# Kernel optimization log

Measured on AMD Instinct MI355X. Metric: run time of the kernel, lower is better.

The kernel has to match this reference:

```python
import jax, jax.numpy as jnp
import numpy as np
from jax import lax

FEATURE_NUM = 16
FILTERS = 64
BATCH = 64
WINDOW = 5
T = 2048
SECTORS = 11
D = 256          # embedding dim / number of quantization buckets
DA = 64
VOCAB = 100000
L = T - 3 * WINDOW + 3  # 2036, length after conv->maxpool->conv (all valid, stride 1)
BN_EPS = 1e-5


def _conv1d(x, w):
    # x: [N, C, W], w: [O, I, K], valid padding, stride 1
    return lax.conv_general_dilated(x, w, (1,), 'VALID', dimension_numbers=('NCH', 'OIH', 'NCH'))


def setup_inputs() -> dict:
    key = jax.random.key(0)
    ks = jax.random.split(key, 9)
    x = jax.random.normal(ks[0], (BATCH, 2 * FEATURE_NUM, T), jnp.float32)
    conv1_w = jax.random.normal(ks[1], (FILTERS, 2 * FEATURE_NUM, WINDOW), jnp.float32) * 0.1
    conv1_b = jnp.zeros((FILTERS,), jnp.float32)
    bn_gamma = jnp.ones((FILTERS,), jnp.float32)
    bn_beta = jnp.zeros((FILTERS,), jnp.float32)
    conv2_w = jax.random.normal(ks[2], (1, FILTERS, WINDOW), jnp.float32) * 0.1
    conv2_b = jnp.zeros((1,), jnp.float32)
    emb = jax.random.normal(ks[3], (VOCAB, D), jnp.float32)
    W1 = jax.random.normal(ks[4], (DA, L), jnp.float32)
    W2 = jax.random.normal(ks[5], (DA, 1), jnp.float32)
    lin_w = jax.random.normal(ks[6], (SECTORS, D), jnp.float32) * 0.05
    lin_b = jnp.zeros((SECTORS,), jnp.float32)
    return {'x': x, 'conv1_w': conv1_w, 'conv1_b': conv1_b, 'bn_gamma': bn_gamma,
            'bn_beta': bn_beta, 'conv2_w': conv2_w, 'conv2_b': conv2_b, 'emb': emb,
            'W1': W1, 'W2': W2, 'lin_w': lin_w, 'lin_b': lin_b}


def reference(x, conv1_w, conv1_b, bn_gamma, bn_beta, conv2_w, conv2_b, emb, W1, W2, lin_w, lin_b):
    # conv1 (valid) -> maxpool(k=WINDOW, s=1) -> batchnorm (train-mode batch stats) -> conv2 -> relu
    h = _conv1d(x, conv1_w) + conv1_b[None, :, None]                     # [B, F, T-W+1]
    h = lax.reduce_window(h, -jnp.inf, lax.max, (1, 1, WINDOW), (1, 1, 1), 'VALID')
    mu = jnp.mean(h, axis=(0, 2), keepdims=True)
    var = jnp.mean((h - mu) ** 2, axis=(0, 2), keepdims=True)            # biased, as torch BN train
    h = (h - mu) * lax.rsqrt(var + BN_EPS) * bn_gamma[None, :, None] + bn_beta[None, :, None]
    h = jax.nn.relu(_conv1d(h, conv2_w) + conv2_b[None, :, None])        # [B, 1, L]
    c = jax.nn.sigmoid(h[:, 0, :])                                       # [B, L] in (0,1)
    # embedding_generate: first j with c <= (j+1)/D  <=>  j = ceil(c*D) - 1
    idx = jnp.clip(jnp.ceil(c * D).astype(jnp.int32) - 1, 0, D - 1)      # [B, L]
    e = emb[idx]                                                         # [B, L, D]
    # per-sample attention: A = W2^T tanh(W1 @ out), batched as einsums
    t = jnp.tanh(jnp.einsum('al,bld->bad', W1, e))                       # [B, DA, D]
    A = jnp.einsum('a,bad->bd', W2[:, 0], t)                             # [B, D]
    att = jax.nn.softmax(jnp.einsum('bld,bd->bl', e, A), axis=1)         # [B, L]
    scores = A @ lin_w.T + lin_b                                         # [B, SECTORS]
    return att, scores
```

## Files before the change

### kernel.cpp

```cpp
#include <hip/hip_runtime.h>
#include <hip/hip_bf16.h>
#include <math.h>

#define BATCH 64
#define CIN   32
#define TIN   2048
#define FILT  64
#define WIN   5
#define TP1   2044
#define TP2   2040
#define LOUT  2036
#define DEMB  256
#define DA    64
#define NSEC  11
#define NC    4
#define CS    509
#define TILE_T 252

__global__ __launch_bounds__(256) void k_prep(
    const float* __restrict__ W1, const float* __restrict__ emb,
    const float* __restrict__ w1, float* __restrict__ w1t,
    float* __restrict__ embT, float* __restrict__ w1r, int* __restrict__ count) {
  __shared__ float tl[64 * 65];
  int bk = blockIdx.x;
  const int tid = threadIdx.x;
  if (bk < 64) { count[bk * 256 + tid] = 0; return; }
  bk -= 64;
  if (bk < 32) {
    const int l0 = bk * 64;
    const int lc = tid & 63, rq = tid >> 6;
    for (int a = rq; a < 64; a += 4)
      tl[a * 65 + lc] = (l0 + lc < LOUT) ? W1[a * LOUT + l0 + lc] : 0.f;
    __syncthreads();
    for (int lp = rq; lp < 64; lp += 4)
      if (l0 + lp < LOUT) w1t[(l0 + lp) * 64 + lc] = tl[lc * 65 + lp];
    return;
  }
  bk -= 32;
  if (bk < 16) {
    const int j0 = (bk & 3) * 64, d0 = (bk >> 2) * 64;
    const int c = tid & 63, rq = tid >> 6;
    for (int j = rq; j < 64; j += 4) tl[j * 65 + c] = emb[(j0 + j) * DEMB + d0 + c];
    __syncthreads();
    for (int d = rq; d < 64; d += 4) embT[(d0 + d) * DEMB + j0 + c] = tl[c * 65 + d];
    return;
  }
  bk -= 16;
  {
    int i = bk * 256 + tid;
    int c = i / 320, r = i - c * 320, f = r / 5, k = r - f * 5;
    w1r[i] = w1[f * (CIN * WIN) + c * WIN + k];
  }
}

__global__ __launch_bounds__(256) void k_conv1pool(
    const float* __restrict__ x, const float* __restrict__ w1r,
    const float* __restrict__ b1, float* __restrict__ h2,
    float* __restrict__ bnps, float* __restrict__ bnpq) {
  __shared__ float wl[CIN * 160];
  const int b   = blockIdx.y;
  const int t0  = blockIdx.x * TILE_T;
  const int tid = threadIdx.x;
  const int z   = blockIdx.z;

  for (int i = tid; i < CIN * 160; i += 256) {
    int c = i / 160, r = i - c * 160;
    wl[i] = w1r[c * 320 + z * 160 + r];
  }
  __syncthreads();

  const int tg   = tid & 63;
  const int tb   = tg * 4;
  const int wv40 = (tid >> 6) * 40;
  const int wf0  = __builtin_amdgcn_readfirstlane(z * 32 + (tid >> 6) * 8);

  float acc[8][4];
#pragma unroll
  for (int ff = 0; ff < 8; ++ff) {
    float bias = b1[wf0 + ff];
    acc[ff][0] = bias; acc[ff][1] = bias; acc[ff][2] = bias; acc[ff][3] = bias;
  }

  const float* xrow = x + (size_t)b * CIN * TIN + t0 + tb;
  const bool safe = (t0 + tb + 8) <= TIN;

  for (int c = 0; c < CIN; ++c) {
    float xw[8];
    if (safe) {
      float4 xa = *(const float4*)(xrow + c * TIN);
      float4 xb = *(const float4*)(xrow + c * TIN + 4);
      xw[0] = xa.x; xw[1] = xa.y; xw[2] = xa.z; xw[3] = xa.w;
      xw[4] = xb.x; xw[5] = xb.y; xw[6] = xb.z; xw[7] = xb.w;
    } else {
#pragma unroll
      for (int j = 0; j < 8; ++j) {
        int gt = t0 + tb + j;
        xw[j] = (gt < TIN) ? xrow[c * TIN + j] : 0.f;
      }
    }
    float wa[40];
#pragma unroll
    for (int q = 0; q < 10; ++q) {
      float4 wq = *(const float4*)&wl[c * 160 + wv40 + q * 4];
      wa[q * 4 + 0] = wq.x; wa[q * 4 + 1] = wq.y;
      wa[q * 4 + 2] = wq.z; wa[q * 4 + 3] = wq.w;
    }
#pragma unroll
    for (int ff = 0; ff < 8; ++ff) {
#pragma unroll
      for (int k = 0; k < WIN; ++k) {
        float wv = wa[ff * 5 + k];
        acc[ff][0] = fmaf(xw[k + 0], wv, acc[ff][0]);
        acc[ff][1] = fmaf(xw[k + 1], wv, acc[ff][1]);
        acc[ff][2] = fmaf(xw[k + 2], wv, acc[ff][2]);
        acc[ff][3] = fmaf(xw[k + 3], wv, acc[ff][3]);
      }
    }
  }

  const bool rowvalid = (tg < 63);
  const int blk = b * 9 + blockIdx.x;
#pragma unroll
  for (int ff = 0; ff < 8; ++ff) {
    float n0 = __shfl_down(acc[ff][0], 1);
    float n1 = __shfl_down(acc[ff][1], 1);
    float n2 = __shfl_down(acc[ff][2], 1);
    float n3 = __shfl_down(acc[ff][3], 1);
    float h[8] = {acc[ff][0], acc[ff][1], acc[ff][2], acc[ff][3], n0, n1, n2, n3};
    float o0 = fmaxf(fmaxf(fmaxf(h[0], h[1]), fmaxf(h[2], h[3])), h[4]);
    float o1 = fmaxf(fmaxf(fmaxf(h[1], h[2]), fmaxf(h[3], h[4])), h[5]);
    float o2 = fmaxf(fmaxf(fmaxf(h[2], h[3]), fmaxf(h[4], h[5])), h[6]);
    float o3 = fmaxf(fmaxf(fmaxf(h[3], h[4]), fmaxf(h[5], h[6])), h[7]);
    const int f = wf0 + ff;
    float s = 0.f, q = 0.f;
    const int t2b = t0 + tb;
    if (rowvalid && (t2b + 3 < TP2)) {
      *(float4*)&h2[((size_t)b * FILT + f) * TP2 + t2b] = make_float4(o0, o1, o2, o3);
      s = o0 + o1 + o2 + o3;
      q = o0 * o0 + o1 * o1 + o2 * o2 + o3 * o3;
    } else if (rowvalid) {
      float ov[4] = {o0, o1, o2, o3};
#pragma unroll
      for (int j = 0; j < 4; ++j) {
        int t2 = t2b + j;
        if (t2 < TP2) { h2[((size_t)b * FILT + f) * TP2 + t2] = ov[j]; s += ov[j]; q += ov[j] * ov[j]; }
      }
    }
#pragma unroll
    for (int off = 32; off > 0; off >>= 1) {
      s += __shfl_down(s, off);
      q += __shfl_down(q, off);
    }
    if (tg == 0) { bnps[blk * FILT + f] = s; bnpq[blk * FILT + f] = q; }
  }
}

__global__ __launch_bounds__(256) void k_bnfin(
    const float* __restrict__ bnps, const float* __restrict__ bnpq,
    const float* __restrict__ gamma, const float* __restrict__ beta,
    const float* __restrict__ w2, const float* __restrict__ b2,
    double* __restrict__ ws2, double* __restrict__ c0p) {
  __shared__ double ls[4 * 64], lq[4 * 64];
  const int tid = threadIdx.x;
  const int f = tid & 63, g = tid >> 6;
  double s = 0.0, q = 0.0;
  for (int blk = g; blk < 576; blk += 4) {
    s += (double)bnps[blk * FILT + f];
    q += (double)bnpq[blk * FILT + f];
  }
  ls[g * 64 + f] = s; lq[g * 64 + f] = q;
  __syncthreads();
  if (tid < 64) {
    s = ls[tid] + ls[64 + tid] + ls[128 + tid] + ls[192 + tid];
    q = lq[tid] + lq[64 + tid] + lq[128 + tid] + lq[192 + tid];
    const double N = (double)(BATCH * TP2);
    double mu  = s / N;
    double var = q / N - mu * mu;
    double sc  = (double)gamma[tid] / sqrt(var + 1e-5);
    double sh  = (double)beta[tid] - mu * sc;
    double wsum = 0.0;
#pragma unroll
    for (int k = 0; k < WIN; ++k) {
      double wv = (double)w2[tid * WIN + k];
      ws2[tid * WIN + k] = sc * wv;
      wsum += wv;
    }
    double part = sh * wsum;
#pragma unroll
    for (int off = 32; off > 0; off >>= 1) part += __shfl_down(part, off);
    if (tid == 0) c0p[0] = part + (double)b2[0];
  }
}

__global__ __launch_bounds__(256) void k_conv2(
    const float* __restrict__ h2, const double* __restrict__ ws2,
    const double* __restrict__ c0p, int* __restrict__ idxp, int* __restrict__ count) {
  __shared__ float hl[FILT * 260];
  __shared__ int hist[DEMB];
  const int b = blockIdx.y;
  const int t0 = blockIdx.x * 256;
  const int tid = threadIdx.x;
  for (int i = tid; i < FILT * 260; i += 256) {
    int f = i / 260, o = i - f * 260;
    int gt = t0 + o;
    hl[i] = (gt < TP2) ? h2[((size_t)b * FILT + f) * TP2 + gt] : 0.f;
  }
  hist[tid] = 0;
  __syncthreads();
  const int t = t0 + tid;
  if (t < LOUT) {
    double z = c0p[0];
    for (int f = 0; f < FILT; ++f) {
      const double* wr = ws2 + f * WIN;
      z = fma((double)hl[f * 260 + tid + 0], wr[0], z);
      z = fma((double)hl[f * 260 + tid + 1], wr[1], z);
      z = fma((double)hl[f * 260 + tid + 2], wr[2], z);
      z = fma((double)hl[f * 260 + tid + 3], wr[3], z);
      z = fma((double)hl[f * 260 + tid + 4], wr[4], z);
    }
    z = z > 0.0 ? z : 0.0;
    double c = 1.0 / (1.0 + exp(-z));
    int iv = (int)ceil(c * 256.0) - 1;
    iv = min(max(iv, 0), DEMB - 1);
    idxp[b * LOUT + t] = iv;
    atomicAdd(&hist[iv], 1);
  }
  __syncthreads();
  atomicAdd(&count[b * DEMB + tid], hist[tid]);
}

__global__ __launch_bounds__(256) void k_sbuild(
    const int* __restrict__ idxp, const float* __restrict__ w1t,
    float* __restrict__ Sg) {
  __shared__ float S[DA * 257];
  __shared__ int il[512];
  const int b = blockIdx.y, ch = blockIdx.x;
  const int tid = threadIdx.x;
  for (int i = tid; i < DA * 257; i += 256) S[i] = 0.f;
  const int l0 = ch * CS;
  for (int i = tid; i < CS; i += 256) il[i] = idxp[b * LOUT + l0 + i];
  __syncthreads();
  const int a = tid & 63, w = tid >> 6;
#pragma unroll 4
  for (int li = w; li < CS; li += 4) {
    int j = il[li];
    float v = w1t[(l0 + li) * DA + a];
    atomicAdd(&S[a * 257 + j], v);
  }
  __syncthreads();
  for (int i = tid; i < DA * DEMB; i += 256) {
    int aa = i >> 8, j = i & 255;
    Sg[((b * NC + ch) * DA + aa) * DEMB + j] = S[aa * 257 + j];
  }
}

__global__ __launch_bounds__(256) void k_gemmA(
    const float* __restrict__ Sg, const float* __restrict__ emb,
    const float* __restrict__ W2, float* __restrict__ Avec) {
  __shared__ float Al[16 * 64];
  __shared__ float Bl[16 * 64];
  __shared__ float red[16 * 64];
  const int b = blockIdx.x, c0 = blockIdx.y * 64;
  const int tid = threadIdx.x;
  const int tx = tid & 15, ty = tid >> 4;
  const int sa = tid >> 2, skq = (tid & 3) * 4;
  const int bk = tid >> 4, bseg = tid & 15;
  float acc[4][4] = {{0}};

  for (int kc = 0; kc < 16; ++kc) {
    const int kb = kc * 16;
    float4 v0 = *(const float4*)&Sg[((b * NC + 0) * DA + sa) * DEMB + kb + skq];
    float4 v1 = *(const float4*)&Sg[((b * NC + 1) * DA + sa) * DEMB + kb + skq];
    float4 v2 = *(const float4*)&Sg[((b * NC + 2) * DA + sa) * DEMB + kb + skq];
    float4 v3 = *(const float4*)&Sg[((b * NC + 3) * DA + sa) * DEMB + kb + skq];
    float4 sv = make_float4(v0.x + v1.x + v2.x + v3.x, v0.y + v1.y + v2.y + v3.y,
                            v0.z + v1.z + v2.z + v3.z, v0.w + v1.w + v2.w + v3.w);
    Al[(skq + 0) * 64 + sa] = sv.x;
    Al[(skq + 1) * 64 + sa] = sv.y;
    Al[(skq + 2) * 64 + sa] = sv.z;
    Al[(skq + 3) * 64 + sa] = sv.w;
    float4 e4 = *(const float4*)&emb[(kb + bk) * DEMB + c0 + bseg * 4];
    *(float4*)&Bl[bk * 64 + bseg * 4] = e4;
    __syncthreads();
#pragma unroll
    for (int k = 0; k < 16; ++k) {
      float4 av = *(const float4*)&Al[k * 64 + ty * 4];
      float4 bv = *(const float4*)&Bl[k * 64 + tx * 4];
      acc[0][0] = fmaf(av.x, bv.x, acc[0][0]); acc[0][1] = fmaf(av.x, bv.y, acc[0][1]);
      acc[0][2] = fmaf(av.x, bv.z, acc[0][2]); acc[0][3] = fmaf(av.x, bv.w, acc[0][3]);
      acc[1][0] = fmaf(av.y, bv.x, acc[1][0]); acc[1][1] = fmaf(av.y, bv.y, acc[1][1]);
      acc[1][2] = fmaf(av.y, bv.z, acc[1][2]); acc[1][3] = fmaf(av.y, bv.w, acc[1][3]);
      acc[2][0] = fmaf(av.z, bv.x, acc[2][0]); acc[2][1] = fmaf(av.z, bv.y, acc[2][1]);
      acc[2][2] = fmaf(av.z, bv.z, acc[2][2]); acc[2][3] = fmaf(av.z, bv.w, acc[2][3]);
      acc[3][0] = fmaf(av.w, bv.x, acc[3][0]); acc[3][1] = fmaf(av.w, bv.y, acc[3][1]);
      acc[3][2] = fmaf(av.w, bv.z, acc[3][2]); acc[3][3] = fmaf(av.w, bv.w, acc[3][3]);
    }
    __syncthreads();
  }
  float cs[4] = {0.f, 0.f, 0.f, 0.f};
#pragma unroll
  for (int r = 0; r < 4; ++r) {
    float wv = W2[ty * 4 + r];
#pragma unroll
    for (int j = 0; j < 4; ++j) cs[j] += tanhf(acc[r][j]) * wv;
  }
#pragma unroll
  for (int j = 0; j < 4; ++j) red[ty * 64 + tx * 4 + j] = cs[j];
  __syncthreads();
  if (tid < 64) {
    float s = 0.f;
#pragma unroll
    for (int q = 0; q < 16; ++q) s += red[q * 64 + tid];
    Avec[b * DEMB + c0 + tid] = s;
  }
}

__global__ __launch_bounds__(256) void k_att(
    const float* __restrict__ Avec, const float* __restrict__ embT,
    const int* __restrict__ count, const float* __restrict__ linw,
    const float* __restrict__ linb, const int* __restrict__ idxp,
    float* __restrict__ att, float* __restrict__ scores) {
  __shared__ float Al[DEMB];
  __shared__ float pl[DEMB];
  __shared__ float scratch[4];
  const int b = blockIdx.x, j = threadIdx.x;
  Al[j] = Avec[b * DEMB + j];
  __syncthreads();
  float dot = 0.f;
  for (int d = 0; d < DEMB; ++d) dot = fmaf(embT[d * DEMB + j], Al[d], dot);
  const int cnt = count[b * DEMB + j];
  float v = (cnt > 0) ? dot : -3.4e38f;
#pragma unroll
  for (int off = 32; off > 0; off >>= 1) v = fmaxf(v, __shfl_down(v, off));
  if ((j & 63) == 0) scratch[j >> 6] = v;
  __syncthreads();
  const float m = fmaxf(fmaxf(scratch[0], scratch[1]), fmaxf(scratch[2], scratch[3]));
  __syncthreads();
  float e = (cnt > 0) ? expf(dot - m) : 0.f;
  float zs = e * (float)cnt;
#pragma unroll
  for (int off = 32; off > 0; off >>= 1) zs += __shfl_down(zs, off);
  if ((j & 63) == 0) scratch[j >> 6] = zs;
  __syncthreads();
  const float Z = scratch[0] + scratch[1] + scratch[2] + scratch[3];
  pl[j] = (cnt > 0) ? e / Z : 0.f;
  __syncthreads();
  for (int l = j; l < LOUT; l += 256)
    att[b * LOUT + l] = pl[idxp[b * LOUT + l]];
  for (int s = 0; s < NSEC; ++s) {
    __syncthreads();
    float part = Al[j] * linw[s * DEMB + j];
#pragma unroll
    for (int off = 32; off > 0; off >>= 1) part += __shfl_down(part, off);
    if ((j & 63) == 0) scratch[j >> 6] = part;
    __syncthreads();
    if (j == 0)
      scores[b * NSEC + s] = scratch[0] + scratch[1] + scratch[2] + scratch[3] + linb[s];
  }
}

extern "C" void kernel_launch(void* const* d_in, const int* in_sizes, int n_in,
                              void* d_out, int out_size, void* d_ws, size_t ws_size,
                              hipStream_t stream) {
  const float* x      = (const float*)d_in[0];
  const float* w1     = (const float*)d_in[1];
  const float* b1     = (const float*)d_in[2];
  const float* gamma  = (const float*)d_in[3];
  const float* beta   = (const float*)d_in[4];
  const float* w2     = (const float*)d_in[5];
  const float* b2     = (const float*)d_in[6];
  const float* emb    = (const float*)d_in[7];
  const float* W1     = (const float*)d_in[8];
  const float* W2     = (const float*)d_in[9];
  const float* linw   = (const float*)d_in[10];
  const float* linb   = (const float*)d_in[11];

  char* ws = (char*)d_ws;
  int*    count = (int*)   (ws + 0);
  double* ws2   = (double*)(ws + 65536);
  double* c0p   = (double*)(ws + 68096);
  float*  bnps  = (float*) (ws + 68608);
  float*  bnpq  = (float*) (ws + 216064);
  int*    idxp  = (int*)   (ws + 363520);
  float*  w1t   = (float*) (ws + 884736);
  float*  embT  = (float*) (ws + 1405952);
  float*  Avec  = (float*) (ws + 1668096);
  float*  w1r   = (float*) (ws + 1733632);
  float*  h2    = (float*) (ws + 1774592);
  float*  Sg    = (float*) (ws + 35197952);

  float* att_out    = (float*)d_out;
  float* scores_out = (float*)d_out + BATCH * LOUT;

  k_prep<<<dim3(152), 256, 0, stream>>>(W1, emb, w1, w1t, embT, w1r, count);
  k_conv1pool<<<dim3(9, 64, 2), 256, 0, stream>>>(x, w1r, b1, h2, bnps, bnpq);
  k_bnfin<<<dim3(1), 256, 0, stream>>>(bnps, bnpq, gamma, beta, w2, b2, ws2, c0p);
  k_conv2<<<dim3(8, 64), 256, 0, stream>>>(h2, ws2, c0p, idxp, count);
  k_sbuild<<<dim3(NC, 64), 256, 0, stream>>>(idxp, w1t, Sg);
  k_gemmA<<<dim3(64, 4), 256, 0, stream>>>(Sg, emb, W2, Avec);
  k_att<<<dim3(64), 256, 0, stream>>>(Avec, embT, count, linw, linb, idxp,
                                      att_out, scores_out);
}
```

Measured before the change: 368.2 us.

## Move BN stats to separate pass, fold BN finalize into conv2, prefetch x

Result: faster. 346.2 us (-6.0%).

```diff
diff --git a/kernel.cpp b/kernel.cpp
--- a/kernel.cpp
+++ b/kernel.cpp
@@ -55,8 +55,7 @@
 
 __global__ __launch_bounds__(256) void k_conv1pool(
     const float* __restrict__ x, const float* __restrict__ w1r,
-    const float* __restrict__ b1, float* __restrict__ h2,
-    float* __restrict__ bnps, float* __restrict__ bnpq) {
+    const float* __restrict__ b1, float* __restrict__ h2) {
   __shared__ float wl[CIN * 160];
   const int b   = blockIdx.y;
   const int t0  = blockIdx.x * TILE_T;
@@ -84,20 +83,27 @@
   const float* xrow = x + (size_t)b * CIN * TIN + t0 + tb;
   const bool safe = (t0 + tb + 8) <= TIN;
 
-  for (int c = 0; c < CIN; ++c) {
-    float xw[8];
+  auto load_x = [&](int c, float* v) {
     if (safe) {
-      float4 xa = *(const float4*)(xrow + c * TIN);
-      float4 xb = *(const float4*)(xrow + c * TIN + 4);
-      xw[0] = xa.x; xw[1] = xa.y; xw[2] = xa.z; xw[3] = xa.w;
-      xw[4] = xb.x; xw[5] = xb.y; xw[6] = xb.z; xw[7] = xb.w;
+      float4 a  = *(const float4*)(xrow + c * TIN);
+      float4 bq = *(const float4*)(xrow + c * TIN + 4);
+      v[0] = a.x;  v[1] = a.y;  v[2] = a.z;  v[3] = a.w;
+      v[4] = bq.x; v[5] = bq.y; v[6] = bq.z; v[7] = bq.w;
     } else {
 #pragma unroll
       for (int j = 0; j < 8; ++j) {
         int gt = t0 + tb + j;
-        xw[j] = (gt < TIN) ? xrow[c * TIN + j] : 0.f;
+        v[j] = (gt < TIN) ? xrow[c * TIN + j] : 0.f;
       }
     }
+  };
+
+  float xw[8];
+  load_x(0, xw);
+#pragma unroll 4
+  for (int c = 0; c < CIN; ++c) {
+    float xn[8];
+    if (c + 1 < CIN) load_x(c + 1, xn);
     float wa[40];
 #pragma unroll
     for (int q = 0; q < 10; ++q) {
@@ -116,10 +122,13 @@
         acc[ff][3] = fmaf(xw[k + 3], wv, acc[ff][3]);
       }
     }
+    if (c + 1 < CIN) {
+#pragma unroll
+      for (int j = 0; j < 8; ++j) xw[j] = xn[j];
+    }
   }
 
   const bool rowvalid = (tg < 63);
-  const int blk = b * 9 + blockIdx.x;
 #pragma unroll
   for (int ff = 0; ff < 8; ++ff) {
     float n0 = __shfl_down(acc[ff][0], 1);
@@ -132,47 +141,67 @@
     float o2 = fmaxf(fmaxf(fmaxf(h[2], h[3]), fmaxf(h[4], h[5])), h[6]);
     float o3 = fmaxf(fmaxf(fmaxf(h[3], h[4]), fmaxf(h[5], h[6])), h[7]);
     const int f = wf0 + ff;
-    float s = 0.f, q = 0.f;
     const int t2b = t0 + tb;
     if (rowvalid && (t2b + 3 < TP2)) {
       *(float4*)&h2[((size_t)b * FILT + f) * TP2 + t2b] = make_float4(o0, o1, o2, o3);
-      s = o0 + o1 + o2 + o3;
-      q = o0 * o0 + o1 * o1 + o2 * o2 + o3 * o3;
     } else if (rowvalid) {
       float ov[4] = {o0, o1, o2, o3};
 #pragma unroll
       for (int j = 0; j < 4; ++j) {
         int t2 = t2b + j;
-        if (t2 < TP2) { h2[((size_t)b * FILT + f) * TP2 + t2] = ov[j]; s += ov[j]; q += ov[j] * ov[j]; }
+        if (t2 < TP2) h2[((size_t)b * FILT + f) * TP2 + t2] = ov[j];
       }
     }
-#pragma unroll
-    for (int off = 32; off > 0; off >>= 1) {
-      s += __shfl_down(s, off);
-      q += __shfl_down(q, off);
-    }
-    if (tg == 0) { bnps[blk * FILT + f] = s; bnpq[blk * FILT + f] = q; }
-  }
-}
-
-__global__ __launch_bounds__(256) void k_bnfin(
-    const float* __restrict__ bnps, const float* __restrict__ bnpq,
-    const float* __restrict__ gamma, const float* __restrict__ beta,
-    const float* __restrict__ w2, const float* __restrict__ b2,
-    double* __restrict__ ws2, double* __restrict__ c0p) {
-  __shared__ double ls[4 * 64], lq[4 * 64];
-  const int tid = threadIdx.x;
-  const int f = tid & 63, g = tid >> 6;
+  }
+}
+
+__global__ __launch_bounds__(256) void k_bnstat(
+    const float* __restrict__ h2, double* __restrict__ bn_s,
+    double* __restrict__ bn_q) {
+  const int g = blockIdx.x, f = blockIdx.y;
+  const int tid = threadIdx.x;
   double s = 0.0, q = 0.0;
-  for (int blk = g; blk < 576; blk += 4) {
-    s += (double)bnps[blk * FILT + f];
-    q += (double)bnpq[blk * FILT + f];
-  }
-  ls[g * 64 + f] = s; lq[g * 64 + f] = q;
-  __syncthreads();
+  for (int bl = 0; bl < 8; ++bl) {
+    const float* row = h2 + ((size_t)(g * 8 + bl) * FILT + f) * TP2;
+    for (int i = tid; i < 510; i += 256) {
+      float4 v = *(const float4*)(row + i * 4);
+      s += (double)v.x + (double)v.y + (double)v.z + (double)v.w;
+      q += (double)v.x * v.x + (double)v.y * v.y +
+           (double)v.z * v.z + (double)v.w * v.w;
+    }
+  }
+#pragma unroll
+  for (int off = 32; off > 0; off >>= 1) {
+    s += __shfl_down(s, off);
+    q += __shfl_down(q, off);
+  }
+  __shared__ double lsd[4], lqd[4];
+  if ((tid & 63) == 0) { lsd[tid >> 6] = s; lqd[tid >> 6] = q; }
+  __syncthreads();
+  if (tid == 0) {
+    bn_s[f * 8 + g] = lsd[0] + lsd[1] + lsd[2] + lsd[3];
+    bn_q[f * 8 + g] = lqd[0] + lqd[1] + lqd[2] + lqd[3];
+  }
+}
+
+__global__ __launch_bounds__(256) void k_conv2(
+    const float* __restrict__ h2, const double* __restrict__ bn_s,
+    const double* __restrict__ bn_q, const float* __restrict__ gamma,
+    const float* __restrict__ beta, const float* __restrict__ w2,
+    const float* __restrict__ b2, int* __restrict__ idxp,
+    int* __restrict__ count) {
+  __shared__ float hl[FILT * 260];
+  __shared__ int hist[DEMB];
+  __shared__ double ws2l[FILT * WIN];
+  __shared__ double c0l;
+  const int b = blockIdx.y;
+  const int t0 = blockIdx.x * 256;
+  const int tid = threadIdx.x;
+
   if (tid < 64) {
-    s = ls[tid] + ls[64 + tid] + ls[128 + tid] + ls[192 + tid];
-    q = lq[tid] + lq[64 + tid] + lq[128 + tid] + lq[192 + tid];
+    double s = 0.0, q = 0.0;
+#pragma unroll
+    for (int g = 0; g < 8; ++g) { s += bn_s[tid * 8 + g]; q += bn_q[tid * 8 + g]; }
     const double N = (double)(BATCH * TP2);
     double mu  = s / N;
     double var = q / N - mu * mu;
@@ -182,24 +211,14 @@
 #pragma unroll
     for (int k = 0; k < WIN; ++k) {
       double wv = (double)w2[tid * WIN + k];
-      ws2[tid * WIN + k] = sc * wv;
+      ws2l[tid * WIN + k] = sc * wv;
       wsum += wv;
     }
     double part = sh * wsum;
 #pragma unroll
     for (int off = 32; off > 0; off >>= 1) part += __shfl_down(part, off);
-    if (tid == 0) c0p[0] = part + (double)b2[0];
-  }
-}
-
-__global__ __launch_bounds__(256) void k_conv2(
-    const float* __restrict__ h2, const double* __restrict__ ws2,
-    const double* __restrict__ c0p, int* __restrict__ idxp, int* __restrict__ count) {
-  __shared__ float hl[FILT * 260];
-  __shared__ int hist[DEMB];
-  const int b = blockIdx.y;
-  const int t0 = blockIdx.x * 256;
-  const int tid = threadIdx.x;
+    if (tid == 0) c0l = part + (double)b2[0];
+  }
   for (int i = tid; i < FILT * 260; i += 256) {
     int f = i / 260, o = i - f * 260;
     int gt = t0 + o;
@@ -209,9 +228,9 @@
   __syncthreads();
   const int t = t0 + tid;
   if (t < LOUT) {
-    double z = c0p[0];
+    double z = c0l;
     for (int f = 0; f < FILT; ++f) {
-      const double* wr = ws2 + f * WIN;
+      const double* wr = &ws2l[f * WIN];
       z = fma((double)hl[f * 260 + tid + 0], wr[0], z);
       z = fma((double)hl[f * 260 + tid + 1], wr[1], z);
       z = fma((double)hl[f * 260 + tid + 2], wr[2], z);
@@ -347,15 +366,15 @@
   __syncthreads();
   for (int l = j; l < LOUT; l += 256)
     att[b * LOUT + l] = pl[idxp[b * LOUT + l]];
-  for (int s = 0; s < NSEC; ++s) {
-    __syncthreads();
-    float part = Al[j] * linw[s * DEMB + j];
+  const int w = j >> 6, lane = j & 63;
+  for (int s = w; s < NSEC; s += 4) {
+    float part = 0.f;
+#pragma unroll
+    for (int r = 0; r < 4; ++r)
+      part = fmaf(Al[lane + r * 64], linw[s * DEMB + lane + r * 64], part);
 #pragma unroll
     for (int off = 32; off > 0; off >>= 1) part += __shfl_down(part, off);
-    if ((j & 63) == 0) scratch[j >> 6] = part;
-    __syncthreads();
-    if (j == 0)
-      scores[b * NSEC + s] = scratch[0] + scratch[1] + scratch[2] + scratch[3] + linb[s];
+    if (lane == 0) scores[b * NSEC + s] = part + linb[s];
   }
 }
 
@@ -377,25 +396,24 @@
 
   char* ws = (char*)d_ws;
   int*    count = (int*)   (ws + 0);
-  double* ws2   = (double*)(ws + 65536);
-  double* c0p   = (double*)(ws + 68096);
-  float*  bnps  = (float*) (ws + 68608);
-  float*  bnpq  = (float*) (ws + 216064);
-  int*    idxp  = (int*)   (ws + 363520);
-  float*  w1t   = (float*) (ws + 884736);
-  float*  embT  = (float*) (ws + 1405952);
-  float*  Avec  = (float*) (ws + 1668096);
-  float*  w1r   = (float*) (ws + 1733632);
-  float*  h2    = (float*) (ws + 1774592);
-  float*  Sg    = (float*) (ws + 35197952);
+  double* bn_s  = (double*)(ws + 65536);
+  double* bn_q  = (double*)(ws + 69632);
+  int*    idxp  = (int*)   (ws + 73728);
+  float*  w1t   = (float*) (ws + 594944);
+  float*  embT  = (float*) (ws + 1116160);
+  float*  Avec  = (float*) (ws + 1378304);
+  float*  w1r   = (float*) (ws + 1443840);
+  float*  h2    = (float*) (ws + 1484800);
+  float*  Sg    = (float*) (ws + 34908160);
 
   float* att_out    = (float*)d_out;
   float* scores_out = (float*)d_out + BATCH * LOUT;
 
   k_prep<<<dim3(152), 256, 0, stream>>>(W1, emb, w1, w1t, embT, w1r, count);
-  k_conv1pool<<<dim3(9, 64, 2), 256, 0, stream>>>(x, w1r, b1, h2, bnps, bnpq);
-  k_bnfin<<<dim3(1), 256, 0, stream>>>(bnps, bnpq, gamma, beta, w2, b2, ws2, c0p);
-  k_conv2<<<dim3(8, 64), 256, 0, stream>>>(h2, ws2, c0p, idxp, count);
+  k_conv1pool<<<dim3(9, 64, 2), 256, 0, stream>>>(x, w1r, b1, h2);
+  k_bnstat<<<dim3(8, 64), 256, 0, stream>>>(h2, bn_s, bn_q);
+  k_conv2<<<dim3(8, 64), 256, 0, stream>>>(h2, bn_s, bn_q, gamma, beta, w2, b2,
+                                           idxp, count);
   k_sbuild<<<dim3(NC, 64), 256, 0, stream>>>(idxp, w1t, Sg);
   k_gemmA<<<dim3(64, 4), 256, 0, stream>>>(Sg, emb, W2, Avec);
   k_att<<<dim3(64), 256, 0, stream>>>(Avec, embT, count, linw, linb, idxp,
```
